# Kernel tuning notes

Hardware: AMD Instinct MI355X
Metric: run time of the kernel (lower is better)

## Reference

```python
import jax, jax.numpy as jnp
import numpy as np
import math

D_MODEL = 256
N_HEAD = 8
D_FF = 1024
WINDOW = 3
RADIUS = 4
NEG = -1e9


def rmsnorm(x, g):
    eps = jnp.asarray(jnp.finfo(x.dtype).eps, x.dtype)
    return x * jax.lax.rsqrt(jnp.mean(x * x, axis=-1, keepdims=True) + eps) * g


def mha(x, Wqkv, bqkv, Wo, bo, mask):
    # x: [B, S, D]; mask: [S, S] bool, True = disallowed
    B, S, D = x.shape
    hd = D // N_HEAD
    qkv = x @ Wqkv.T + bqkv
    q, k, v = jnp.split(qkv, 3, axis=-1)
    q = q.reshape(B, S, N_HEAD, hd).transpose(0, 2, 1, 3)
    k = k.reshape(B, S, N_HEAD, hd).transpose(0, 2, 1, 3)
    v = v.reshape(B, S, N_HEAD, hd).transpose(0, 2, 1, 3)
    scores = jnp.einsum('bhqd,bhkd->bhqk', q, k) / math.sqrt(hd)
    scores = jnp.where(mask[None, None], jnp.asarray(NEG, scores.dtype), scores)
    attn = jax.nn.softmax(scores, axis=-1)
    o = jnp.einsum('bhqk,bhkd->bhqd', attn, v)
    o = o.transpose(0, 2, 1, 3).reshape(B, S, D)
    return o @ Wo.T + bo


def setup_inputs() -> dict:
    key = jax.random.key(0)
    ks = jax.random.split(key, 16)
    d, dff = D_MODEL, D_FF
    sc = 0.02
    inp = {
        'x': jax.random.normal(ks[0], (4, 16384, d), dtype=jnp.float32),
        'coords': jax.random.randint(ks[1], (128, 2), 0, 12),
        'spatial_size': 128,
        'Wqkv_s': jax.random.normal(ks[2], (3 * d, d), jnp.float32) * sc,
        'bqkv_s': jnp.zeros((3 * d,), jnp.float32),
        'Wo_s': jax.random.normal(ks[3], (d, d), jnp.float32) * sc,
        'bo_s': jnp.zeros((d,), jnp.float32),
        'Wqkv_t': jax.random.normal(ks[4], (3 * d, d), jnp.float32) * sc,
        'bqkv_t': jnp.zeros((3 * d,), jnp.float32),
        'Wo_t': jax.random.normal(ks[5], (d, d), jnp.float32) * sc,
        'bo_t': jnp.zeros((d,), jnp.float32),
        'g1': jnp.ones((d,), jnp.float32),
        'g2': jnp.ones((d,), jnp.float32),
        'g3': jnp.ones((d,), jnp.float32),
        'W1': jax.random.normal(ks[6], (dff, d), jnp.float32) * sc,
        'b1': jnp.zeros((dff,), jnp.float32),
        'W2': jax.random.normal(ks[7], (d, dff), jnp.float32) * sc,
        'b2': jnp.zeros((d,), jnp.float32),
    }
    return inp


def reference(x, coords, spatial_size, Wqkv_s, bqkv_s, Wo_s, bo_s,
              Wqkv_t, bqkv_t, Wo_t, bo_t, g1, g2, g3, W1, b1, W2, b2):
    b, seq, d = x.shape
    s = int(spatial_size)
    t = seq // s

    # spatial mask: Chebyshev distance between 2D coords > RADIUS -> masked
    dx = jnp.abs(coords[:, 0][:, None] - coords[:, 0][None, :])
    dy = jnp.abs(coords[:, 1][:, None] - coords[:, 1][None, :])
    smask = jnp.maximum(dx, dy) > RADIUS  # [s, s]

    # temporal mask: attend only to keys j with 0 <= i - j <= WINDOW
    idx = jnp.arange(t)
    dd = idx[:, None] - idx[None, :]
    tmask = ~((dd >= 0) & (dd <= WINDOW))  # [t, t]

    x4 = x.reshape(b, t, s, d)

    # spatial attention over s within each (b, t)
    xs = x4.reshape(b * t, s, d)
    y_s = mha(rmsnorm(xs, g1), Wqkv_s, bqkv_s, Wo_s, bo_s, smask)
    x4 = x4 + y_s.reshape(b, t, s, d)

    # temporal attention over t within each (b, s)
    x_t = x4.transpose(0, 2, 1, 3).reshape(b * s, t, d)
    y_t = mha(rmsnorm(x_t, g2), Wqkv_t, bqkv_t, Wo_t, bo_t, tmask)
    x4 = x4 + y_t.reshape(b, s, t, d).transpose(0, 2, 1, 3)

    # FFN (exact GELU, matching torch nn.GELU default)
    h = rmsnorm(x4, g3)
    y = jax.nn.gelu(h @ W1.T + b1, approximate=False) @ W2.T + b2
    x4 = x4 + y
    return x4.reshape(b, seq, d)
```

## Files before the change

kernel.cpp:

```cpp
#include <hip/hip_runtime.h>
#include <hip/hip_bf16.h>

typedef __attribute__((ext_vector_type(4))) float f32x4;
typedef __attribute__((ext_vector_type(8))) short bf16x8;
typedef __attribute__((ext_vector_type(4))) unsigned short u16x4;

#define NTOK 65536
#define DMODEL 256
#define DFF 1024
#define NH 8
#define HD 32
#define SSP 128
#define TLEN 128
#define SCALE 0.17677669529663687f

__device__ __forceinline__ float bf2f(unsigned short u) {
    return __builtin_bit_cast(float, (unsigned int)u << 16);
}
__device__ __forceinline__ unsigned short f2bf(float f) {
    unsigned int u = __builtin_bit_cast(unsigned int, f);
    unsigned int r = u + 0x7fffu + ((u >> 16) & 1u);
    return (unsigned short)(r >> 16);
}
__device__ __forceinline__ void gload_lds16(const void* g, void* l) {
    __builtin_amdgcn_global_load_lds((const __attribute__((address_space(1))) void*)g,
                                     (__attribute__((address_space(3))) void*)l, 16, 0, 0);
}

__global__ __launch_bounds__(256)
void cvt_w(const float* __restrict__ a, const float* __restrict__ b,
           const float* __restrict__ c, const float* __restrict__ d,
           const float* __restrict__ e, const float* __restrict__ f,
           unsigned short* __restrict__ o)
{
    int i = blockIdx.x * 256 + threadIdx.x;
    float v;
    if      (i < 196608)  v = a[i];
    else if (i < 262144)  v = b[i - 196608];
    else if (i < 458752)  v = c[i - 262144];
    else if (i < 524288)  v = d[i - 458752];
    else if (i < 786432)  v = e[i - 524288];
    else                  v = f[i - 786432];
    o[i] = f2bf(v);
}

__global__ __launch_bounds__(256)
void rmsnorm_k(const float* __restrict__ x, const float* __restrict__ g,
               unsigned short* __restrict__ out)
{
    const int row = blockIdx.x * 4 + (threadIdx.x >> 6);
    const int lane = threadIdx.x & 63;
    const float4 v = *(const float4*)&x[(size_t)row * DMODEL + lane * 4];
    float s = v.x * v.x + v.y * v.y + v.z * v.z + v.w * v.w;
    #pragma unroll
    for (int o = 1; o < 64; o <<= 1) s += __shfl_xor(s, o);
    const float rinv = rsqrtf(s * (1.0f / DMODEL) + 1.1920929e-7f);
    const float4 gv = *(const float4*)&g[lane * 4];
    u16x4 o4;
    o4[0] = f2bf(v.x * rinv * gv.x);
    o4[1] = f2bf(v.y * rinv * gv.y);
    o4[2] = f2bf(v.z * rinv * gv.z);
    o4[3] = f2bf(v.w * rinv * gv.w);
    *(u16x4*)&out[(size_t)row * DMODEL + lane * 4] = o4;
}

template<int EPI>
__global__ __launch_bounds__(256)
void gemm_bt(const unsigned short* __restrict__ A,
             const unsigned short* __restrict__ W,
             const float* __restrict__ bias,
             unsigned short* __restrict__ Cb,
             float* __restrict__ Cf,
             int N, int K, int NCT)
{
    __shared__ unsigned short lds[17408];
    unsigned short* As = lds;
    unsigned short* Bs = lds + 8192;

    const int tid = threadIdx.x;
    const int wave = tid >> 6, lane = tid & 63;
    const int wr = wave >> 1, wc = wave & 1;

    const int nwg = gridDim.x;
    const int bid = blockIdx.x;
    const int lin = (bid & 7) * (nwg >> 3) + (bid >> 3);
    const int row0 = (lin / NCT) * 128;
    const int col0 = (lin % NCT) * 128;

    f32x4 acc[4][4];
    #pragma unroll
    for (int i = 0; i < 4; i++)
        #pragma unroll
        for (int j = 0; j < 4; j++)
            acc[i][j] = (f32x4){0.f, 0.f, 0.f, 0.f};

    const int srow  = tid >> 3;
    const int kx    = ((tid & 7) * 8) ^ ((srow & 7) * 8);

    const int fr = lane & 15, g = lane >> 4;
    const int sw = (fr & 7) * 8;

    for (int k0 = 0; k0 < K; k0 += 64) {
        #pragma unroll
        for (int q = 0; q < 4; q++) {
            const int row = q * 32 + srow;
            gload_lds16(A + (size_t)(row0 + row) * K + k0 + kx, As + q * 2048 + tid * 8);
            gload_lds16(W + (size_t)(col0 + row) * K + k0 + kx, Bs + q * 2048 + tid * 8);
        }
        __syncthreads();
        #pragma unroll
        for (int kh = 0; kh < 2; kh++) {
            const int ke = (kh * 32 + g * 8) ^ sw;
            bf16x8 af[4], bw[4];
            #pragma unroll
            for (int i = 0; i < 4; i++)
                af[i] = *(const bf16x8*)&As[(wr * 64 + i * 16 + fr) * 64 + ke];
            #pragma unroll
            for (int j = 0; j < 4; j++)
                bw[j] = *(const bf16x8*)&Bs[(wc * 64 + j * 16 + fr) * 64 + ke];
            #pragma unroll
            for (int i = 0; i < 4; i++)
                #pragma unroll
                for (int j = 0; j < 4; j++)
                    acc[i][j] = __builtin_amdgcn_mfma_f32_16x16x32_bf16(af[i], bw[j], acc[i][j], 0, 0, 0);
        }
        __syncthreads();
    }

    if constexpr (EPI == 2) {
        #pragma unroll
        for (int i = 0; i < 4; i++) {
            #pragma unroll
            for (int j = 0; j < 4; j++) {
                const int col = col0 + wc * 64 + j * 16 + fr;
                const float bv = bias[col];
                #pragma unroll
                for (int r = 0; r < 4; r++) {
                    const int row = row0 + wr * 64 + i * 16 + g * 4 + r;
                    Cf[(size_t)row * N + col] += acc[i][j][r] + bv;
                }
            }
        }
    } else {
        #pragma unroll
        for (int i = 0; i < 4; i++) {
            #pragma unroll
            for (int j = 0; j < 4; j++) {
                const int col = wc * 64 + j * 16 + fr;
                const float bv = bias[col0 + col];
                #pragma unroll
                for (int r = 0; r < 4; r++) {
                    float v = acc[i][j][r] + bv;
                    if constexpr (EPI == 1) v = 0.5f * v * (1.0f + erff(v * 0.70710678118654752f));
                    lds[(wr * 64 + i * 16 + g * 4 + r) * 136 + col] = f2bf(v);
                }
            }
        }
        __syncthreads();
        #pragma unroll
        for (int q = 0; q < 8; q++) {
            const int chunk = q * 256 + tid;
            const int row = chunk >> 4, c16 = chunk & 15;
            *(bf16x8*)&Cb[(size_t)(row0 + row) * N + col0 + c16 * 8] =
                *(const bf16x8*)&lds[row * 136 + c16 * 8];
        }
    }
}

__global__ __launch_bounds__(256)
void attn_spatial(const unsigned short* __restrict__ qkv,
                  const int* __restrict__ coords,
                  unsigned short* __restrict__ out)
{
    __shared__ unsigned short Qs[128 * 32];
    __shared__ unsigned short Ks[128 * 32];
    __shared__ unsigned short Vt[32 * 136];
    __shared__ unsigned short Pb[64 * 132];
    __shared__ int cx[128], cy[128];

    const int bt = blockIdx.x, h = blockIdx.y;
    const int tid = threadIdx.x, wave = tid >> 6, lane = tid & 63;
    const size_t base = (size_t)bt * SSP * 768 + (size_t)h * HD;

    {
        const int rr = tid >> 1, cb = (tid & 1) * 16;
        const unsigned short* p = qkv + base + (size_t)rr * 768 + cb;
        *(bf16x8*)&Qs[rr * 32 + cb]     = *(const bf16x8*)p;
        *(bf16x8*)&Qs[rr * 32 + cb + 8] = *(const bf16x8*)(p + 8);
        p += 256;
        *(bf16x8*)&Ks[rr * 32 + cb]     = *(const bf16x8*)p;
        *(bf16x8*)&Ks[rr * 32 + cb + 8] = *(const bf16x8*)(p + 8);
        p += 256;
        bf16x8 v0 = *(const bf16x8*)p, v1 = *(const bf16x8*)(p + 8);
        #pragma unroll
        for (int e = 0; e < 8; e++) {
            Vt[(cb + e) * 136 + rr]     = (unsigned short)v0[e];
            Vt[(cb + 8 + e) * 136 + rr] = (unsigned short)v1[e];
        }
        if (tid < 128) { cx[tid] = coords[2 * tid]; cy[tid] = coords[2 * tid + 1]; }
    }
    __syncthreads();

    const int fr = lane & 15;
    const int g  = lane >> 4;
    const int fko = g * 8;

    for (int half = 0; half < 2; half++) {
        const int rbase = half * 64 + wave * 16;
        bf16x8 aq = *(const bf16x8*)&Qs[(rbase + fr) * 32 + fko];
        f32x4 sc[8];
        #pragma unroll
        for (int tj = 0; tj < 8; tj++) {
            bf16x8 bk = *(const bf16x8*)&Ks[(tj * 16 + fr) * 32 + fko];
            sc[tj] = __builtin_amdgcn_mfma_f32_16x16x32_bf16(aq, bk, (f32x4){0.f,0.f,0.f,0.f}, 0, 0, 0);
        }
        int cxi[4], cyi[4];
        #pragma unroll
        for (int r = 0; r < 4; r++) { const int i = rbase + g * 4 + r; cxi[r] = cx[i]; cyi[r] = cy[i]; }
        float m[4] = {-1e30f, -1e30f, -1e30f, -1e30f};
        #pragma unroll
        for (int tj = 0; tj < 8; tj++) {
            const int j = tj * 16 + fr;
            const int cxj = cx[j], cyj = cy[j];
            #pragma unroll
            for (int r = 0; r < 4; r++) {
                int dx = cxi[r] - cxj; dx = dx < 0 ? -dx : dx;
                int dy = cyi[r] - cyj; dy = dy < 0 ? -dy : dy;
                const float v = ((dx > dy ? dx : dy) > 4) ? -1e9f : sc[tj][r] * SCALE;
                sc[tj][r] = v;
                m[r] = fmaxf(m[r], v);
            }
        }
        #pragma unroll
        for (int r = 0; r < 4; r++) {
            #pragma unroll
            for (int o = 1; o < 16; o <<= 1) m[r] = fmaxf(m[r], __shfl_xor(m[r], o));
        }
        float sm[4] = {0.f, 0.f, 0.f, 0.f};
        #pragma unroll
        for (int tj = 0; tj < 8; tj++) {
            #pragma unroll
            for (int r = 0; r < 4; r++) {
                const float e = __expf(sc[tj][r] - m[r]);
                sc[tj][r] = e;
                sm[r] += e;
            }
        }
        #pragma unroll
        for (int r = 0; r < 4; r++) {
            #pragma unroll
            for (int o = 1; o < 16; o <<= 1) sm[r] += __shfl_xor(sm[r], o);
        }
        float inv[4];
        #pragma unroll
        for (int r = 0; r < 4; r++) inv[r] = 1.0f / sm[r];
        #pragma unroll
        for (int tj = 0; tj < 8; tj++) {
            #pragma unroll
            for (int r = 0; r < 4; r++)
                Pb[(wave * 16 + g * 4 + r) * 132 + tj * 16 + fr] = f2bf(sc[tj][r] * inv[r]);
        }
        #pragma unroll
        for (int td = 0; td < 2; td++) {
            f32x4 o = (f32x4){0.f, 0.f, 0.f, 0.f};
            #pragma unroll
            for (int kk = 0; kk < 4; kk++) {
                bf16x8 pa = *(const bf16x8*)&Pb[(wave * 16 + fr) * 132 + kk * 32 + fko];
                bf16x8 bv = *(const bf16x8*)&Vt[(td * 16 + fr) * 136 + kk * 32 + fko];
                o = __builtin_amdgcn_mfma_f32_16x16x32_bf16(pa, bv, o, 0, 0, 0);
            }
            #pragma unroll
            for (int r = 0; r < 4; r++) {
                const int i = half * 64 + wave * 16 + g * 4 + r;
                const int d = td * 16 + fr;
                out[((size_t)(bt * SSP + i)) * DMODEL + h * HD + d] = f2bf(o[r]);
            }
        }
    }
}

__device__ __forceinline__ float dot32(const float* __restrict__ qr,
                                       const unsigned short* __restrict__ Kt, int j)
{
    float a = 0.f;
    #pragma unroll
    for (int d = 0; d < 32; d++) a += qr[d] * bf2f(Kt[d * 128 + j]);
    return a;
}

__global__ __launch_bounds__(128)
void attn_temporal(const unsigned short* __restrict__ qkv,
                   unsigned short* __restrict__ out)
{
    __shared__ unsigned short Qt[32 * 128], Kt[32 * 128], Vt[32 * 128];
    const int bs = blockIdx.x, h = blockIdx.y;
    const int b = bs >> 7, sp = bs & 127;
    const int tid = threadIdx.x;
    const size_t rb = ((size_t)b * 16384 + (size_t)tid * 128 + sp) * 768 + (size_t)h * HD;
    #pragma unroll
    for (int c = 0; c < 4; c++) {
        bf16x8 q = *(const bf16x8*)(qkv + rb + c * 8);
        bf16x8 k = *(const bf16x8*)(qkv + rb + 256 + c * 8);
        bf16x8 v = *(const bf16x8*)(qkv + rb + 512 + c * 8);
        #pragma unroll
        for (int e = 0; e < 8; e++) {
            const int d = c * 8 + e;
            Qt[d * 128 + tid] = (unsigned short)q[e];
            Kt[d * 128 + tid] = (unsigned short)k[e];
            Vt[d * 128 + tid] = (unsigned short)v[e];
        }
    }
    __syncthreads();

    const int i = tid;
    float qr[32];
    #pragma unroll
    for (int d = 0; d < 32; d++) qr[d] = bf2f(Qt[d * 128 + i]);

    float s0 = -1e30f, s1 = -1e30f, s2 = -1e30f;
    if (i >= 3) s0 = dot32(qr, Kt, i - 3) * SCALE;
    if (i >= 2) s1 = dot32(qr, Kt, i - 2) * SCALE;
    if (i >= 1) s2 = dot32(qr, Kt, i - 1) * SCALE;
    const float s3 = dot32(qr, Kt, i) * SCALE;

    const float mx = fmaxf(fmaxf(s0, s1), fmaxf(s2, s3));
    const float p0 = __expf(s0 - mx), p1 = __expf(s1 - mx), p2 = __expf(s2 - mx), p3 = __expf(s3 - mx);
    const float inv = 1.0f / (p0 + p1 + p2 + p3);
    const int j0 = i >= 3 ? i - 3 : 0;
    const int j1 = i >= 2 ? i - 2 : 0;
    const int j2 = i >= 1 ? i - 1 : 0;
    const size_t ob = ((size_t)b * 16384 + (size_t)i * 128 + sp) * DMODEL + (size_t)h * HD;
    #pragma unroll
    for (int d = 0; d < 32; d++) {
        const float o = (p0 * bf2f(Vt[d * 128 + j0]) + p1 * bf2f(Vt[d * 128 + j1]) +
                         p2 * bf2f(Vt[d * 128 + j2]) + p3 * bf2f(Vt[d * 128 + i])) * inv;
        out[ob + d] = f2bf(o);
    }
}

extern "C" void kernel_launch(void* const* d_in, const int* in_sizes, int n_in,
                              void* d_out, int out_size, void* d_ws, size_t ws_size,
                              hipStream_t stream)
{
    const int*   coords = (const int*)d_in[1];
    const float* Wqkv_s = (const float*)d_in[3];
    const float* bqkv_s = (const float*)d_in[4];
    const float* Wo_s   = (const float*)d_in[5];
    const float* bo_s   = (const float*)d_in[6];
    const float* Wqkv_t = (const float*)d_in[7];
    const float* bqkv_t = (const float*)d_in[8];
    const float* Wo_t   = (const float*)d_in[9];
    const float* bo_t   = (const float*)d_in[10];
    const float* g1     = (const float*)d_in[11];
    const float* g2     = (const float*)d_in[12];
    const float* g3     = (const float*)d_in[13];
    const float* W1     = (const float*)d_in[14];
    const float* b1     = (const float*)d_in[15];
    const float* W2     = (const float*)d_in[16];
    const float* b2     = (const float*)d_in[17];
    float* xo = (float*)d_out;

    char* ws = (char*)d_ws;
    unsigned short* wb  = (unsigned short*)ws;
    unsigned short* xn  = (unsigned short*)(ws + (size_t)2 * 1024 * 1024);
    unsigned short* big = (unsigned short*)(ws + (size_t)34 * 1024 * 1024);

    unsigned short* wQKVs = wb;
    unsigned short* wOs   = wb + 196608;
    unsigned short* wQKVt = wb + 262144;
    unsigned short* wOt   = wb + 458752;
    unsigned short* w1b   = wb + 524288;
    unsigned short* w2b   = wb + 786432;

    (void)hipMemcpyAsync(d_out, d_in[0], (size_t)NTOK * DMODEL * sizeof(float),
                         hipMemcpyDeviceToDevice, stream);
    cvt_w<<<4096, 256, 0, stream>>>(Wqkv_s, Wo_s, Wqkv_t, Wo_t, W1, W2, wb);

    rmsnorm_k<<<16384, 256, 0, stream>>>(xo, g1, xn);
    gemm_bt<0><<<3072, 256, 0, stream>>>(xn, wQKVs, bqkv_s, big, nullptr, 768, 256, 6);
    attn_spatial<<<dim3(512, 8), 256, 0, stream>>>(big, coords, xn);
    gemm_bt<2><<<1024, 256, 0, stream>>>(xn, wOs, bo_s, nullptr, xo, 256, 256, 2);

    rmsnorm_k<<<16384, 256, 0, stream>>>(xo, g2, xn);
    gemm_bt<0><<<3072, 256, 0, stream>>>(xn, wQKVt, bqkv_t, big, nullptr, 768, 256, 6);
    attn_temporal<<<dim3(512, 8), 128, 0, stream>>>(big, xn);
    gemm_bt<2><<<1024, 256, 0, stream>>>(xn, wOt, bo_t, nullptr, xo, 256, 256, 2);

    rmsnorm_k<<<16384, 256, 0, stream>>>(xo, g3, xn);
    gemm_bt<1><<<4096, 256, 0, stream>>>(xn, w1b, b1, big, nullptr, 1024, 256, 8);
    gemm_bt<2><<<1024, 256, 0, stream>>>(big, w2b, b2, nullptr, xo, 256, 1024, 2);
}
```

Measured before the change: 642.6 us.

## Fuse residual add and RMSNorm into out-projection GEMM, drop input memcpy

Adds a gemm_rms kernel in which each block owns 64 full rows. It computes the attention out-projection, adds the result into the residual, and reduces row sums of squares across waves through LDS to emit the next normalized bf16 activation. This removes two standalone RMSNorm passes. The input copy into the output buffer is folded into the first RMSNorm kernel, exact erf GELU is replaced by a tanh-form sigmoid approximation, and the temporal attention keeps Q in registers instead of LDS. The GELU change alters numerics slightly, and the fused GEMM writes xn in place over its own input rows after its K loop finishes.

```diff
diff --git a/kernel.cpp b/kernel.cpp
--- a/kernel.cpp
+++ b/kernel.cpp
@@ -45,8 +45,8 @@
 }
 
 __global__ __launch_bounds__(256)
-void rmsnorm_k(const float* __restrict__ x, const float* __restrict__ g,
-               unsigned short* __restrict__ out)
+void rms_copy(const float* __restrict__ x, const float* __restrict__ g,
+              float* __restrict__ xo, unsigned short* __restrict__ xn)
 {
     const int row = blockIdx.x * 4 + (threadIdx.x >> 6);
     const int lane = threadIdx.x & 63;
@@ -55,13 +55,14 @@
     #pragma unroll
     for (int o = 1; o < 64; o <<= 1) s += __shfl_xor(s, o);
     const float rinv = rsqrtf(s * (1.0f / DMODEL) + 1.1920929e-7f);
+    *(float4*)&xo[(size_t)row * DMODEL + lane * 4] = v;
     const float4 gv = *(const float4*)&g[lane * 4];
     u16x4 o4;
     o4[0] = f2bf(v.x * rinv * gv.x);
     o4[1] = f2bf(v.y * rinv * gv.y);
     o4[2] = f2bf(v.z * rinv * gv.z);
     o4[3] = f2bf(v.w * rinv * gv.w);
-    *(u16x4*)&out[(size_t)row * DMODEL + lane * 4] = o4;
+    *(u16x4*)&xn[(size_t)row * DMODEL + lane * 4] = o4;
 }
 
 template<int EPI>
@@ -151,7 +152,10 @@
                 #pragma unroll
                 for (int r = 0; r < 4; r++) {
                     float v = acc[i][j][r] + bv;
-                    if constexpr (EPI == 1) v = 0.5f * v * (1.0f + erff(v * 0.70710678118654752f));
+                    if constexpr (EPI == 1) {
+                        const float y = 1.5957691216057308f * (v + 0.044715f * v * v * v);
+                        v = v / (1.0f + __expf(-y));
+                    }
                     lds[(wr * 64 + i * 16 + g * 4 + r) * 136 + col] = f2bf(v);
                 }
             }
@@ -163,6 +167,109 @@
             const int row = chunk >> 4, c16 = chunk & 15;
             *(bf16x8*)&Cb[(size_t)(row0 + row) * N + col0 + c16 * 8] =
                 *(const bf16x8*)&lds[row * 136 + c16 * 8];
+        }
+    }
+}
+
+__global__ __launch_bounds__(256)
+void gemm_rms(const unsigned short* __restrict__ A,
+              const unsigned short* __restrict__ W,
+              const float* __restrict__ bias,
+              float* __restrict__ xo,
+              const float* __restrict__ gv,
+              unsigned short* __restrict__ xn,
+              int K)
+{
+    __shared__ unsigned short As[64 * 64];
+    __shared__ unsigned short Bs[256 * 64];
+    __shared__ float red[64 * 4];
+
+    const int tid = threadIdx.x;
+    const int wave = tid >> 6, lane = tid & 63;
+    const int fr = lane & 15, g4 = lane >> 4;
+
+    const int nwg = gridDim.x;
+    const int bid = blockIdx.x;
+    const int lin = (bid & 7) * (nwg >> 3) + (bid >> 3);
+    const int row0 = lin * 64;
+
+    f32x4 acc[4][4];
+    #pragma unroll
+    for (int i = 0; i < 4; i++)
+        #pragma unroll
+        for (int j = 0; j < 4; j++)
+            acc[i][j] = (f32x4){0.f, 0.f, 0.f, 0.f};
+
+    const int srow = tid >> 3;
+    const int kx   = ((tid & 7) * 8) ^ ((srow & 7) * 8);
+    const int sw   = (fr & 7) * 8;
+
+    for (int k0 = 0; k0 < K; k0 += 64) {
+        #pragma unroll
+        for (int p = 0; p < 2; p++)
+            gload_lds16(A + (size_t)(row0 + p * 32 + srow) * K + k0 + kx, As + p * 2048 + tid * 8);
+        #pragma unroll
+        for (int p = 0; p < 8; p++)
+            gload_lds16(W + (size_t)(p * 32 + srow) * K + k0 + kx, Bs + p * 2048 + tid * 8);
+        __syncthreads();
+        #pragma unroll
+        for (int kh = 0; kh < 2; kh++) {
+            const int ke = (kh * 32 + g4 * 8) ^ sw;
+            bf16x8 af[4], bw[4];
+            #pragma unroll
+            for (int i = 0; i < 4; i++)
+                af[i] = *(const bf16x8*)&As[(i * 16 + fr) * 64 + ke];
+            #pragma unroll
+            for (int j = 0; j < 4; j++)
+                bw[j] = *(const bf16x8*)&Bs[(wave * 64 + j * 16 + fr) * 64 + ke];
+            #pragma unroll
+            for (int i = 0; i < 4; i++)
+                #pragma unroll
+                for (int j = 0; j < 4; j++)
+                    acc[i][j] = __builtin_amdgcn_mfma_f32_16x16x32_bf16(af[i], bw[j], acc[i][j], 0, 0, 0);
+        }
+        __syncthreads();
+    }
+
+    #pragma unroll
+    for (int i = 0; i < 4; i++) {
+        #pragma unroll
+        for (int j = 0; j < 4; j++) {
+            const int col = wave * 64 + j * 16 + fr;
+            const float bv = bias[col];
+            #pragma unroll
+            for (int r = 0; r < 4; r++) {
+                const int row = row0 + i * 16 + g4 * 4 + r;
+                const float xv = xo[(size_t)row * DMODEL + col] + acc[i][j][r] + bv;
+                xo[(size_t)row * DMODEL + col] = xv;
+                acc[i][j][r] = xv;
+            }
+        }
+    }
+    #pragma unroll
+    for (int i = 0; i < 4; i++) {
+        #pragma unroll
+        for (int r = 0; r < 4; r++) {
+            float p = acc[i][0][r] * acc[i][0][r] + acc[i][1][r] * acc[i][1][r]
+                    + acc[i][2][r] * acc[i][2][r] + acc[i][3][r] * acc[i][3][r];
+            #pragma unroll
+            for (int o = 1; o < 16; o <<= 1) p += __shfl_xor(p, o);
+            if (fr == 0) red[(i * 16 + g4 * 4 + r) * 4 + wave] = p;
+        }
+    }
+    __syncthreads();
+    #pragma unroll
+    for (int i = 0; i < 4; i++) {
+        #pragma unroll
+        for (int r = 0; r < 4; r++) {
+            const int rl = i * 16 + g4 * 4 + r;
+            const float rsq = red[rl * 4 + 0] + red[rl * 4 + 1] + red[rl * 4 + 2] + red[rl * 4 + 3];
+            const float rinv = rsqrtf(rsq * (1.0f / DMODEL) + 1.1920929e-7f);
+            #pragma unroll
+            for (int j = 0; j < 4; j++) {
+                const int col = wave * 64 + j * 16 + fr;
+                xn[(size_t)(row0 + rl) * DMODEL + col] = f2bf(acc[i][j][r] * rinv * gv[col]);
+            }
         }
     }
 }
@@ -292,20 +399,20 @@
 void attn_temporal(const unsigned short* __restrict__ qkv,
                    unsigned short* __restrict__ out)
 {
-    __shared__ unsigned short Qt[32 * 128], Kt[32 * 128], Vt[32 * 128];
+    __shared__ unsigned short Kt[32 * 128], Vt[32 * 128];
     const int bs = blockIdx.x, h = blockIdx.y;
     const int b = bs >> 7, sp = bs & 127;
     const int tid = threadIdx.x;
     const size_t rb = ((size_t)b * 16384 + (size_t)tid * 128 + sp) * 768 + (size_t)h * HD;
+    bf16x8 qreg[4];
     #pragma unroll
     for (int c = 0; c < 4; c++) {
-        bf16x8 q = *(const bf16x8*)(qkv + rb + c * 8);
+        qreg[c] = *(const bf16x8*)(qkv + rb + c * 8);
         bf16x8 k = *(const bf16x8*)(qkv + rb + 256 + c * 8);
         bf16x8 v = *(const bf16x8*)(qkv + rb + 512 + c * 8);
         #pragma unroll
         for (int e = 0; e < 8; e++) {
             const int d = c * 8 + e;
-            Qt[d * 128 + tid] = (unsigned short)q[e];
             Kt[d * 128 + tid] = (unsigned short)k[e];
             Vt[d * 128 + tid] = (unsigned short)v[e];
         }
@@ -315,7 +422,7 @@
     const int i = tid;
     float qr[32];
     #pragma unroll
-    for (int d = 0; d < 32; d++) qr[d] = bf2f(Qt[d * 128 + i]);
+    for (int d = 0; d < 32; d++) qr[d] = bf2f((unsigned short)qreg[d >> 3][d & 7]);
 
     float s0 = -1e30f, s1 = -1e30f, s2 = -1e30f;
     if (i >= 3) s0 = dot32(qr, Kt, i - 3) * SCALE;
@@ -342,6 +449,7 @@
                               void* d_out, int out_size, void* d_ws, size_t ws_size,
                               hipStream_t stream)
 {
+    const float* x_in   = (const float*)d_in[0];
     const int*   coords = (const int*)d_in[1];
     const float* Wqkv_s = (const float*)d_in[3];
     const float* bqkv_s = (const float*)d_in[4];
@@ -372,21 +480,17 @@
     unsigned short* w1b   = wb + 524288;
     unsigned short* w2b   = wb + 786432;
 
-    (void)hipMemcpyAsync(d_out, d_in[0], (size_t)NTOK * DMODEL * sizeof(float),
-                         hipMemcpyDeviceToDevice, stream);
     cvt_w<<<4096, 256, 0, stream>>>(Wqkv_s, Wo_s, Wqkv_t, Wo_t, W1, W2, wb);
 
-    rmsnorm_k<<<16384, 256, 0, stream>>>(xo, g1, xn);
+    rms_copy<<<16384, 256, 0, stream>>>(x_in, g1, xo, xn);
     gemm_bt<0><<<3072, 256, 0, stream>>>(xn, wQKVs, bqkv_s, big, nullptr, 768, 256, 6);
     attn_spatial<<<dim3(512, 8), 256, 0, stream>>>(big, coords, xn);
-    gemm_bt<2><<<1024, 256, 0, stream>>>(xn, wOs, bo_s, nullptr, xo, 256, 256, 2);
-
-    rmsnorm_k<<<16384, 256, 0, stream>>>(xo, g2, xn);
+    gemm_rms<<<1024, 256, 0, stream>>>(xn, wOs, bo_s, xo, g2, xn, 256);
+
     gemm_bt<0><<<3072, 256, 0, stream>>>(xn, wQKVt, bqkv_t, big, nullptr, 768, 256, 6);
     attn_temporal<<<dim3(512, 8), 128, 0, stream>>>(big, xn);
-    gemm_bt<2><<<1024, 256, 0, stream>>>(xn, wOt, bo_t, nullptr, xo, 256, 256, 2);
-
-    rmsnorm_k<<<16384, 256, 0, stream>>>(xo, g3, xn);
+    gemm_rms<<<1024, 256, 0, stream>>>(xn, wOt, bo_t, xo, g3, xn, 256);
+
     gemm_bt<1><<<4096, 256, 0, stream>>>(xn, w1b, b1, big, nullptr, 1024, 256, 8);
     gemm_bt<2><<<1024, 256, 0, stream>>>(big, w2b, b2, nullptr, xo, 256, 1024, 2);
 }
```

Result: no change. 641.1 us (-0.2%).
